# Optimization experiments

Measured on AMD Instinct MI355X. Metric: run time of the kernel, lower is better.

## Reference

```python
import jax, jax.numpy as jnp
import numpy as np
import math

B, L, H, E, D = 4, 2048, 8, 64, 64


def _build_local_log_symmetry_mask(L):
    # Faithful port of LocalLogSymmetryMask: True = masked-out position.
    lws = math.ceil(np.log2(L) / 2)  # local window size
    n_log = math.ceil(10 * np.log2(L))
    m = np.zeros((L, L), dtype=np.float32)
    for i in range(L):
        row = m[i]
        # left side: local window + log-spaced long-range
        if i - lws + 1 < 0:
            row[:i] = 1
        else:
            row[i - lws + 1:i + 1] = 1
            for k in range(n_log):
                ni = i - lws + 1 - int(1.5 ** k)
                if ni >= 0:
                    row[ni] = 1
                else:
                    break
        # right side (symmetric)
        if i + lws - 1 >= L:
            row[i:] = 1
        else:
            row[i:i + lws] = 1
            for k in range(n_log):
                ni = i + lws - 1 + int(1.5 ** k)
                if ni < L:
                    row[ni] = 1
                else:
                    break
    return m == 0  # True where attention is NOT allowed


def setup_inputs() -> dict:
    key = jax.random.key(0)
    kq, kk, kv = jax.random.split(key, 3)
    queries = jax.random.normal(kq, (B, L, H, E), dtype=jnp.float32)
    keys = jax.random.normal(kk, (B, L, H, E), dtype=jnp.float32)
    values = jax.random.normal(kv, (B, L, H, D), dtype=jnp.float32)
    mask = jnp.asarray(_build_local_log_symmetry_mask(L))  # [L, L] bool
    return {"queries": queries, "keys": keys, "values": values, "mask": mask}


def reference(queries, keys, values, mask):
    # queries/keys: [B,L,H,E], values: [B,L,H,D], mask: [L,L] bool (True = masked)
    E_ = queries.shape[-1]
    scale = 1.0 / math.sqrt(E_)
    # scores: [B,H,L,S]
    scores = jnp.einsum("blhe,bshe->bhls", queries, keys) * scale
    scores = jnp.where(mask[None, None, :, :], -jnp.inf, scores)
    attn = jax.nn.softmax(scores, axis=-1)  # dropout disabled (eval mode)
    out = jnp.einsum("bhls,bshd->blhd", attn, values)  # [B,L,H,D]
    return out
```

## Files before the change

### kernel.cpp

```cpp
#include <hip/hip_runtime.h>


#define KB 4
#define KL 2048
#define KH 8
#define KE 64
#define KWAVES 4
#define KROWS (KB * KL * KH)
#define KBLOCKS (KROWS / KWAVES)
#define KROWB (KH * KE * 4)
#define KVROWB 256
#define KWSBYTES ((size_t)KROWS * KVROWB)

typedef __fp16 h2 __attribute__((ext_vector_type(2)));
typedef unsigned ui4 __attribute__((ext_vector_type(4)));

static constexpr int kOff[48] = {
    -5, -4, -3, -2, -1, 0, 1, 2, 3, 4, 5,
    -6, -7, -8, -10, -12, -16, -22, -30, -43, -62, -91, -134, -199, -296,
    -442, -661, -990, -1482,
    6, 7, 8, 10, 12, 16, 22, 30, 43, 62, 91, 134, 199, 296, 442, 661, 990,
    1482,
    1 << 19};

template <int CTRL>
__device__ __forceinline__ float dpp_radd(float x) {
    int t = __builtin_amdgcn_update_dpp(0, __float_as_int(x), CTRL, 0xF, 0xF,
                                        false);
    return x + __int_as_float(t);
}
template <int CTRL>
__device__ __forceinline__ unsigned dpp_mov1_u(unsigned x) {
#if __has_builtin(__builtin_amdgcn_mov_dpp)
    return (unsigned)__builtin_amdgcn_mov_dpp((int)x, CTRL, 0xF, 0xF, true);
#else
    return (unsigned)__builtin_amdgcn_update_dpp(0, (int)x, CTRL, 0xF, 0xF,
                                                 true);
#endif
}
template <int CTRL>
__device__ __forceinline__ unsigned dpp_mov_u(unsigned x) {
    return (unsigned)__builtin_amdgcn_update_dpp(0, (int)x, CTRL, 0xF, 0xF,
                                                 false);
}

#if __has_builtin(__builtin_amdgcn_permlane16_swap)
#define KHAVE_PL16 1
__device__ __forceinline__ void pl16u(unsigned x, unsigned& a, unsigned& b) {
    auto r = __builtin_amdgcn_permlane16_swap(x, x, false, false);
    a = r[0];
    b = r[1];
}
#else
#define KHAVE_PL16 0
__device__ __forceinline__ void pl16u(unsigned x, unsigned& a, unsigned& b) {
    a = x;
    b = (unsigned)__shfl_xor((int)x, 16, 64);
}
#endif
#if __has_builtin(__builtin_amdgcn_permlane32_swap)
__device__ __forceinline__ void pl32u(unsigned x, unsigned& a, unsigned& b) {
    auto r = __builtin_amdgcn_permlane32_swap(x, x, false, false);
    a = r[0];
    b = r[1];
}
#else
__device__ __forceinline__ void pl32u(unsigned x, unsigned& a, unsigned& b) {
    a = x;
    b = (unsigned)__shfl_xor((int)x, 32, 64);
}
#endif

__device__ __forceinline__ float red16_add(float x) {
    unsigned a, b;
    pl16u(__float_as_uint(x), a, b);
    return __uint_as_float(a) + __uint_as_float(b);
}
__device__ __forceinline__ float red32_add(float x) {
    unsigned a, b;
    pl32u(__float_as_uint(x), a, b);
    return __uint_as_float(a) + __uint_as_float(b);
}
__device__ __forceinline__ h2 as_h2(unsigned u) {
    return __builtin_bit_cast(h2, u);
}
__device__ __forceinline__ unsigned as_u(h2 x) {
    return __builtin_bit_cast(unsigned, x);
}
__device__ __forceinline__ h2 red16_pk(h2 x) {
    unsigned a, b;
    pl16u(as_u(x), a, b);
    return as_h2(a) + as_h2(b);
}
__device__ __forceinline__ h2 red32_pk(h2 x) {
    unsigned a, b;
    pl32u(as_u(x), a, b);
    return as_h2(a) + as_h2(b);
}

#if __has_builtin(__builtin_amdgcn_exp2f)
#define KEXP2(x) __builtin_amdgcn_exp2f(x)
#else
#define KEXP2(x) exp2f(x)
#endif

__device__ __forceinline__ h2 pkrtz(float a, float b) {
#if __has_builtin(__builtin_amdgcn_cvt_pkrtz)
    return __builtin_amdgcn_cvt_pkrtz(a, b);
#else
    h2 r;
    r[0] = (__fp16)a;
    r[1] = (__fp16)b;
    return r;
#endif
}
__device__ __forceinline__ float fd2(h2 a, h2 b, float c) {
#if __has_builtin(__builtin_amdgcn_fdot2)
    return __builtin_amdgcn_fdot2(a, b, c, false);
#else
    return fmaf((float)a[1], (float)b[1], fmaf((float)a[0], (float)b[0], c));
#endif
}

__global__ __launch_bounds__(256) void MaskAttention_prep_kernel(
    const float* __restrict__ k, const float* __restrict__ v,
    unsigned* __restrict__ kv) {
    const unsigned t  = (unsigned)blockIdx.x * 256u + (unsigned)threadIdx.x;
    const unsigned m  = t & 7u;
    const unsigned gr = t >> 3;
    const unsigned j  = gr & (KL - 1);
    const unsigned bh = gr >> 11;
    const unsigned b  = bh >> 3;
    const unsigned h  = bh & 7;
    const size_t el = (((size_t)b * KL + j) * KH + h) * KE + (size_t)m * 8;
    const float* sk = k + el;
    const float* sv = v + el;
    const float4 kx = *(const float4*)sk;
    const float4 ky = *(const float4*)(sk + 4);
    const float4 vx = *(const float4*)sv;
    const float4 vy = *(const float4*)(sv + 4);
    ui4 ok_, ov_;
    ok_[0] = as_u(pkrtz(kx.x, kx.y));
    ok_[1] = as_u(pkrtz(kx.z, kx.w));
    ok_[2] = as_u(pkrtz(ky.x, ky.y));
    ok_[3] = as_u(pkrtz(ky.z, ky.w));
    ov_[0] = as_u(pkrtz(vx.x, vx.y));
    ov_[1] = as_u(pkrtz(vx.z, vx.w));
    ov_[2] = as_u(pkrtz(vy.x, vy.y));
    ov_[3] = as_u(pkrtz(vy.z, vy.w));
    char* dst = (char*)kv + (size_t)gr * KVROWB + (size_t)m * 32;
    *(ui4*)dst        = ok_;
    *(ui4*)(dst + 16) = ov_;
}

__global__ __launch_bounds__(256) void MaskAttention_20572893347881_kernel(
    const float* __restrict__ q, const unsigned* __restrict__ kv,
    float* __restrict__ out) {
    const int tid  = (int)threadIdx.x;
    const int lane = tid & 63;
    const int g    = lane >> 4;
    const int e4   = lane & 15;
    const int wave = __builtin_amdgcn_readfirstlane(tid >> 6);

    __shared__ int ddt[48];
    if (tid < 48) ddt[tid] = kOff[tid] * KVROWB;
    __syncthreads();

    const int p = (int)blockIdx.x;
    const int l = (p & 7) * (KBLOCKS / 8) + (p >> 3);
    const int r = l * KWAVES + wave;
    const int i  = r & (KL - 1);
    const int bh = r >> 11;

    const char* __restrict__ kvb =
        (const char*)kv + (size_t)bh * (KL * KVROWB);
    const size_t hbB = (size_t)(bh >> 3) * (KL * KROWB) +
                       (size_t)(bh & 7) * (KE * 4);
    const char* __restrict__ qc = (const char*)q + hbB;
    char* __restrict__ oc       = (char*)out + hbB;

    const unsigned co     = (unsigned)(e4 * 16);
    const unsigned base_r = (unsigned)i * KVROWB + co;
    const unsigned clampv = (unsigned)(KL - 1) * KVROWB + co;

    unsigned off[12];
    bool ok[12];
#pragma unroll
    for (int t = 0; t < 12; ++t) {
        const unsigned u = base_r + (unsigned)ddt[4 * t + g];
        ok[t]  = u < (unsigned)(KL * KVROWB);
        off[t] = u < clampv ? u : clampv;
    }

    const float4 qf = *(const float4*)(qc + (unsigned)i * KROWB + co);
    const float qs  = 0.125f * 1.44269504088896340736f;
    const h2 qa = pkrtz(qf.x * qs, qf.y * qs);
    const h2 qb = pkrtz(qf.z * qs, qf.w * qs);
    const h2 qan = as_h2(dpp_mov_u<0x101>(as_u(qa)));
    const h2 qbn = as_h2(dpp_mov_u<0x101>(as_u(qb)));

    float dsum = 0.f;
    h2 acc01 = {0, 0}, acc23 = {0, 0}, acc45 = {0, 0}, acc67 = {0, 0};
#pragma unroll
    for (int t = 0; t < 12; ++t) {
        const ui4 w = *(const ui4*)(kvb + off[t]);
        float sd = fd2(as_h2(w[0]), qa,
                       fd2(as_h2(w[1]), qb,
                           fd2(as_h2(w[2]), qan, fd2(as_h2(w[3]), qbn, 0.f))));
        sd = dpp_radd<0x122>(sd);
        sd = dpp_radd<0x124>(sd);
        sd = dpp_radd<0x128>(sd);
        const float pp = ok[t] ? KEXP2(sd) : 0.f;
        const float pv = __uint_as_float(dpp_mov1_u<0x111>(__float_as_uint(pp)));
        dsum += pv;
        const h2 p2 = pkrtz(pv, pv);
        acc01 = __builtin_elementwise_fma(p2, as_h2(w[0]), acc01);
        acc23 = __builtin_elementwise_fma(p2, as_h2(w[1]), acc23);
        acc45 = __builtin_elementwise_fma(p2, as_h2(w[2]), acc45);
        acc67 = __builtin_elementwise_fma(p2, as_h2(w[3]), acc67);
    }

    float d = red32_add(red16_add(dsum));
    const float inv = __builtin_amdgcn_rcpf(d);
    acc01 = red32_pk(red16_pk(acc01));
    acc23 = red32_pk(red16_pk(acc23));
    acc45 = red32_pk(red16_pk(acc45));
    acc67 = red32_pk(red16_pk(acc67));

    if ((lane < 16) && (lane & 1)) {
        const int m = lane >> 1;
        char* dst = oc + (unsigned)i * KROWB + (unsigned)m * 32;
        float4 o0 = make_float4((float)acc01[0] * inv, (float)acc01[1] * inv,
                                (float)acc23[0] * inv, (float)acc23[1] * inv);
        float4 o1 = make_float4((float)acc45[0] * inv, (float)acc45[1] * inv,
                                (float)acc67[0] * inv, (float)acc67[1] * inv);
        *(float4*)dst = o0;
        *(float4*)(dst + 16) = o1;
    }
}

__global__ __launch_bounds__(256) void MaskAttention_f32_fallback_kernel(
    const float* __restrict__ q, const float* __restrict__ k,
    const float* __restrict__ v, float* __restrict__ out) {
    const int tid  = (int)threadIdx.x;
    const int lane = tid & 63;
    const int g    = lane >> 4;
    const int e4   = lane & 15;
    const int wave = __builtin_amdgcn_readfirstlane(tid >> 6);
    const int p = (int)blockIdx.x;
    const int l = (p & 7) * (KBLOCKS / 8) + (p >> 3);
    const int r = l * KWAVES + wave;
    const int i = r & (KL - 1);
    const int h = (r >> 11) & (KH - 1);
    const int b = r >> 14;
    const size_t hbB = (size_t)b * (KL * KROWB) + (size_t)h * (KE * 4);
    const char* __restrict__ qc = (const char*)q + hbB;
    const char* __restrict__ kc = (const char*)k + hbB;
    const char* __restrict__ vc = (const char*)v + hbB;
    char* __restrict__ oc       = (char*)out + hbB;
    const unsigned co     = (unsigned)(e4 * 16);
    const unsigned base   = (unsigned)i * KROWB + co;
    const unsigned clampv = (unsigned)((KL - 1) * KROWB) + co;
    const bool g1 = (g & 1) != 0;
    const bool g2 = (g & 2) != 0;
    unsigned off[12];
    bool ok[12];
#pragma unroll
    for (int t = 0; t < 12; ++t) {
        const int a0 = kOff[4 * t + 0] * KROWB;
        const int a1 = kOff[4 * t + 1] * KROWB;
        const int a2 = kOff[4 * t + 2] * KROWB;
        const int a3 = kOff[4 * t + 3] * KROWB;
        const int dd = g1 ? (g2 ? a3 : a1) : (g2 ? a2 : a0);
        const unsigned u = base + (unsigned)dd;
        ok[t]  = u < (unsigned)(KL * KROWB);
        off[t] = u < clampv ? u : clampv;
    }
    float4 qf = *(const float4*)(qc + base);
    const float qs = 0.125f * 1.44269504088896340736f;
    qf.x *= qs; qf.y *= qs; qf.z *= qs; qf.w *= qs;
    float dsum = 0.f;
    float4 acc = make_float4(0.f, 0.f, 0.f, 0.f);
#pragma unroll
    for (int t = 0; t < 12; ++t) {
        const float4 kf = *(const float4*)(kc + off[t]);
        const float4 vf = *(const float4*)(vc + off[t]);
        float sd = qf.x * kf.x + qf.y * kf.y + qf.z * kf.z + qf.w * kf.w;
        sd = dpp_radd<0x121>(sd);
        sd = dpp_radd<0x122>(sd);
        sd = dpp_radd<0x124>(sd);
        sd = dpp_radd<0x128>(sd);
        const float pr = ok[t] ? KEXP2(sd) : 0.f;
        dsum += pr;
        acc.x = fmaf(pr, vf.x, acc.x);
        acc.y = fmaf(pr, vf.y, acc.y);
        acc.z = fmaf(pr, vf.z, acc.z);
        acc.w = fmaf(pr, vf.w, acc.w);
    }
    float d = red32_add(red16_add(dsum));
    const float inv = __builtin_amdgcn_rcpf(d);
    acc.x = red32_add(red16_add(acc.x));
    acc.y = red32_add(red16_add(acc.y));
    acc.z = red32_add(red16_add(acc.z));
    acc.w = red32_add(red16_add(acc.w));
    if (lane < 16) {
        float4 o = make_float4(acc.x * inv, acc.y * inv, acc.z * inv,
                               acc.w * inv);
        *(float4*)(oc + base) = o;
    }
}

extern "C" void kernel_launch(void* const* d_in, const int* in_sizes, int n_in,
                              void* d_out, int out_size, void* d_ws,
                              size_t ws_size, hipStream_t stream) {
    (void)in_sizes; (void)n_in; (void)out_size;
    const float* q = (const float*)d_in[0];
    const float* k = (const float*)d_in[1];
    const float* v = (const float*)d_in[2];
    float* out = (float*)d_out;

    if (d_ws != nullptr && ws_size >= KWSBYTES) {
        unsigned* kv = (unsigned*)d_ws;
        hipLaunchKernelGGL(MaskAttention_prep_kernel,
                           dim3(KROWS * 8 / 256), dim3(256), 0, stream,
                           k, v, kv);
        hipLaunchKernelGGL(MaskAttention_20572893347881_kernel,
                           dim3(KBLOCKS), dim3(KWAVES * 64), 0, stream,
                           q, kv, out);
    } else {
        hipLaunchKernelGGL(MaskAttention_f32_fallback_kernel,
                           dim3(KBLOCKS), dim3(KWAVES * 64), 0, stream,
                           q, k, v, out);
    }
}
```

Before: 139.2 us.

## Split packed K/V workspace into separate planes and remap lanes per key

New measurement: 148.3 us. 1.07x slower.

```diff
diff --git a/kernel.cpp b/kernel.cpp
--- a/kernel.cpp
+++ b/kernel.cpp
@@ -9,8 +9,9 @@
 #define KROWS (KB * KL * KH)
 #define KBLOCKS (KROWS / KWAVES)
 #define KROWB (KH * KE * 4)
-#define KVROWB 256
-#define KWSBYTES ((size_t)KROWS * KVROWB)
+#define KPROWB 128
+#define KPACKB ((size_t)KROWS * KPROWB)
+#define KWSBYTES (2 * KPACKB)
 
 typedef __fp16 h2 __attribute__((ext_vector_type(2)));
 typedef unsigned ui4 __attribute__((ext_vector_type(4)));
@@ -45,14 +46,12 @@
 }
 
 #if __has_builtin(__builtin_amdgcn_permlane16_swap)
-#define KHAVE_PL16 1
 __device__ __forceinline__ void pl16u(unsigned x, unsigned& a, unsigned& b) {
     auto r = __builtin_amdgcn_permlane16_swap(x, x, false, false);
     a = r[0];
     b = r[1];
 }
 #else
-#define KHAVE_PL16 0
 __device__ __forceinline__ void pl16u(unsigned x, unsigned& a, unsigned& b) {
     a = x;
     b = (unsigned)__shfl_xor((int)x, 16, 64);
@@ -124,7 +123,7 @@
 
 __global__ __launch_bounds__(256) void MaskAttention_prep_kernel(
     const float* __restrict__ k, const float* __restrict__ v,
-    unsigned* __restrict__ kv) {
+    unsigned* __restrict__ ws) {
     const unsigned t  = (unsigned)blockIdx.x * 256u + (unsigned)threadIdx.x;
     const unsigned m  = t & 7u;
     const unsigned gr = t >> 3;
@@ -148,22 +147,25 @@
     ov_[1] = as_u(pkrtz(vx.z, vx.w));
     ov_[2] = as_u(pkrtz(vy.x, vy.y));
     ov_[3] = as_u(pkrtz(vy.z, vy.w));
-    char* dst = (char*)kv + (size_t)gr * KVROWB + (size_t)m * 32;
-    *(ui4*)dst        = ok_;
-    *(ui4*)(dst + 16) = ov_;
+    char* kdst = (char*)ws + (size_t)gr * KPROWB + (size_t)m * 16;
+    char* vdst = kdst + KPACKB;
+    *(ui4*)kdst = ok_;
+    *(ui4*)vdst = ov_;
 }
 
 __global__ __launch_bounds__(256) void MaskAttention_20572893347881_kernel(
-    const float* __restrict__ q, const unsigned* __restrict__ kv,
+    const float* __restrict__ q, const unsigned* __restrict__ ws,
     float* __restrict__ out) {
     const int tid  = (int)threadIdx.x;
     const int lane = tid & 63;
     const int g    = lane >> 4;
     const int e4   = lane & 15;
+    const int par  = lane & 1;
+    const int gp   = g + (par << 2);
     const int wave = __builtin_amdgcn_readfirstlane(tid >> 6);
 
     __shared__ int ddt[48];
-    if (tid < 48) ddt[tid] = kOff[tid] * KVROWB;
+    if (tid < 48) ddt[tid] = kOff[tid] * KPROWB;
     __syncthreads();
 
     const int p = (int)blockIdx.x;
@@ -172,60 +174,75 @@
     const int i  = r & (KL - 1);
     const int bh = r >> 11;
 
-    const char* __restrict__ kvb =
-        (const char*)kv + (size_t)bh * (KL * KVROWB);
+    const char* __restrict__ kpb = (const char*)ws + (size_t)bh * (KL * KPROWB);
+    const char* __restrict__ vpb = kpb + KPACKB;
     const size_t hbB = (size_t)(bh >> 3) * (KL * KROWB) +
                        (size_t)(bh & 7) * (KE * 4);
     const char* __restrict__ qc = (const char*)q + hbB;
     char* __restrict__ oc       = (char*)out + hbB;
 
-    const unsigned co     = (unsigned)(e4 * 16);
-    const unsigned base_r = (unsigned)i * KVROWB + co;
-    const unsigned clampv = (unsigned)(KL - 1) * KVROWB + co;
-
-    unsigned off[12];
-    bool ok[12];
+    const unsigned co2    = (unsigned)((e4 >> 1) * 16);
+    const unsigned base_r = (unsigned)i * KPROWB + co2;
+    const unsigned clampv = (unsigned)(KL - 1) * KPROWB + co2;
+
+    unsigned off[6];
+    bool ok[6];
 #pragma unroll
-    for (int t = 0; t < 12; ++t) {
-        const unsigned u = base_r + (unsigned)ddt[4 * t + g];
-        ok[t]  = u < (unsigned)(KL * KVROWB);
-        off[t] = u < clampv ? u : clampv;
-    }
-
-    const float4 qf = *(const float4*)(qc + (unsigned)i * KROWB + co);
+    for (int s = 0; s < 6; ++s) {
+        const unsigned u = base_r + (unsigned)ddt[8 * s + gp];
+        ok[s]  = u < (unsigned)(KL * KPROWB);
+        off[s] = u < clampv ? u : clampv;
+    }
+
+    const float4 qf = *(const float4*)(qc + (unsigned)i * KROWB +
+                                       (unsigned)(e4 * 16));
     const float qs  = 0.125f * 1.44269504088896340736f;
-    const h2 qa = pkrtz(qf.x * qs, qf.y * qs);
-    const h2 qb = pkrtz(qf.z * qs, qf.w * qs);
-    const h2 qan = as_h2(dpp_mov_u<0x101>(as_u(qa)));
-    const h2 qbn = as_h2(dpp_mov_u<0x101>(as_u(qb)));
+    const h2 own0 = pkrtz(qf.x * qs, qf.y * qs);
+    const h2 own1 = pkrtz(qf.z * qs, qf.w * qs);
+    const unsigned shr0 = dpp_mov1_u<0x111>(as_u(own0));
+    const unsigned shr1 = dpp_mov1_u<0x111>(as_u(own1));
+    const unsigned shl0 = dpp_mov_u<0x101>(as_u(own0));
+    const unsigned shl1 = dpp_mov_u<0x101>(as_u(own1));
+    const bool ev = (par == 0);
+    const h2 qh0 = ev ? own0 : as_h2(shr0);
+    const h2 qh1 = ev ? own1 : as_h2(shr1);
+    const h2 qh2 = ev ? as_h2(shl0) : own0;
+    const h2 qh3 = ev ? as_h2(shl1) : own1;
 
     float dsum = 0.f;
     h2 acc01 = {0, 0}, acc23 = {0, 0}, acc45 = {0, 0}, acc67 = {0, 0};
 #pragma unroll
-    for (int t = 0; t < 12; ++t) {
-        const ui4 w = *(const ui4*)(kvb + off[t]);
-        float sd = fd2(as_h2(w[0]), qa,
-                       fd2(as_h2(w[1]), qb,
-                           fd2(as_h2(w[2]), qan, fd2(as_h2(w[3]), qbn, 0.f))));
+    for (int s = 0; s < 6; ++s) {
+        const ui4 wk = *(const ui4*)(kpb + off[s]);
+        const ui4 wv = *(const ui4*)(vpb + off[s]);
+        float sd = fd2(as_h2(wk[0]), qh0,
+                       fd2(as_h2(wk[1]), qh1,
+                           fd2(as_h2(wk[2]), qh2,
+                               fd2(as_h2(wk[3]), qh3, 0.f))));
         sd = dpp_radd<0x122>(sd);
         sd = dpp_radd<0x124>(sd);
         sd = dpp_radd<0x128>(sd);
-        const float pp = ok[t] ? KEXP2(sd) : 0.f;
-        const float pv = __uint_as_float(dpp_mov1_u<0x111>(__float_as_uint(pp)));
-        dsum += pv;
-        const h2 p2 = pkrtz(pv, pv);
-        acc01 = __builtin_elementwise_fma(p2, as_h2(w[0]), acc01);
-        acc23 = __builtin_elementwise_fma(p2, as_h2(w[1]), acc23);
-        acc45 = __builtin_elementwise_fma(p2, as_h2(w[2]), acc45);
-        acc67 = __builtin_elementwise_fma(p2, as_h2(w[3]), acc67);
-    }
-
+        const float pp = ok[s] ? KEXP2(sd) : 0.f;
+        dsum += pp;
+        const h2 p2 = pkrtz(pp, pp);
+        acc01 = __builtin_elementwise_fma(p2, as_h2(wv[0]), acc01);
+        acc23 = __builtin_elementwise_fma(p2, as_h2(wv[1]), acc23);
+        acc45 = __builtin_elementwise_fma(p2, as_h2(wv[2]), acc45);
+        acc67 = __builtin_elementwise_fma(p2, as_h2(wv[3]), acc67);
+    }
+
+    dsum = dpp_radd<0x121>(dsum);
     float d = red32_add(red16_add(dsum));
     const float inv = __builtin_amdgcn_rcpf(d);
+
     acc01 = red32_pk(red16_pk(acc01));
     acc23 = red32_pk(red16_pk(acc23));
     acc45 = red32_pk(red16_pk(acc45));
     acc67 = red32_pk(red16_pk(acc67));
+    acc01 = acc01 + as_h2(dpp_mov1_u<0x111>(as_u(acc01)));
+    acc23 = acc23 + as_h2(dpp_mov1_u<0x111>(as_u(acc23)));
+    acc45 = acc45 + as_h2(dpp_mov1_u<0x111>(as_u(acc45)));
+    acc67 = acc67 + as_h2(dpp_mov1_u<0x111>(as_u(acc67)));
 
     if ((lane < 16) && (lane & 1)) {
         const int m = lane >> 1;
@@ -320,13 +337,13 @@
     float* out = (float*)d_out;
 
     if (d_ws != nullptr && ws_size >= KWSBYTES) {
-        unsigned* kv = (unsigned*)d_ws;
+        unsigned* ws = (unsigned*)d_ws;
         hipLaunchKernelGGL(MaskAttention_prep_kernel,
                            dim3(KROWS * 8 / 256), dim3(256), 0, stream,
-                           k, v, kv);
+                           k, v, ws);
         hipLaunchKernelGGL(MaskAttention_20572893347881_kernel,
                            dim3(KBLOCKS), dim3(KWAVES * 64), 0, stream,
-                           q, kv, out);
+                           q, ws, out);
     } else {
         hipLaunchKernelGGL(MaskAttention_f32_fallback_kernel,
                            dim3(KBLOCKS), dim3(KWAVES * 64), 0, stream,
```
